# Optimization experiments

Measured on AMD Instinct MI355X. Metric: run time of the kernel, lower is better.

## Reference

```python
import jax, jax.numpy as jnp
import numpy as np

B, C, H, W = 8, 192, 120, 120
WSIZES = [4, 8, 12]
BN_EPS = 1e-5


def _conv1x1(t, w, b):
    # t: [b,c,h,w], w: [o,c], b: [o]
    return jnp.einsum('oc,bchw->bohw', w, t) + b[None, :, None, None]


def _bn(t, g, bb, m, v):
    scale = (g * jax.lax.rsqrt(v + BN_EPS))[None, :, None, None]
    return (t - m[None, :, None, None]) * scale + bb[None, :, None, None]


def _partition_qv(t, ws):
    # t: [b, 2c, h, w] -> qx, vx each [b*nh*nw, ws*ws, c]
    b, c2, h, w = t.shape
    c = c2 // 2
    nh, nw = h // ws, w // ws
    t = t.reshape(b, 2, c, nh, ws, nw, ws)
    t = t.transpose(1, 0, 3, 5, 4, 6, 2).reshape(2, b * nh * nw, ws * ws, c)
    return t[0], t[1]


def _merge(t, ws, b, h, w):
    # t: [b*nh*nw, ws*ws, c] -> [b, c, h, w]
    nh, nw = h // ws, w // ws
    c = t.shape[-1]
    t = t.reshape(b, nh, nw, ws, ws, c)
    return t.transpose(0, 5, 1, 3, 2, 4).reshape(b, c, h, w)


def setup_inputs() -> dict:
    key = jax.random.key(0)
    ks = jax.random.split(key, 6)
    d = {}
    d['x'] = jax.random.normal(ks[0], (B, C, H, W), jnp.float32)
    d['y'] = jax.random.normal(ks[1], (B, C, H, W), jnp.float32)
    d['w_in'] = jax.random.normal(ks[2], (2 * C, C), jnp.float32) * 0.05
    d['b_in'] = jax.random.normal(ks[3], (2 * C,), jnp.float32) * 0.01
    d['bn_gamma'] = jnp.ones((2 * C,), jnp.float32)
    d['bn_beta'] = jnp.zeros((2 * C,), jnp.float32)
    d['bn_mean'] = jnp.zeros((2 * C,), jnp.float32)
    d['bn_var'] = jnp.ones((2 * C,), jnp.float32)
    d['w_out'] = jax.random.normal(ks[4], (C, C), jnp.float32) * 0.05
    d['b_out'] = jax.random.normal(ks[5], (C,), jnp.float32) * 0.01
    return d


def reference(x, y, w_in, b_in, bn_gamma, bn_beta, bn_mean, bn_var, w_out, b_out):
    b, c, h, w = x.shape
    xp = _bn(_conv1x1(x, w_in, b_in), bn_gamma, bn_beta, bn_mean, bn_var)
    yp = _bn(_conv1x1(y, w_in, b_in), bn_gamma, bn_beta, bn_mean, bn_var)
    chunk = c * 2 // 3
    y1s, atns = [], []
    for i, ws in enumerate(WSIZES):
        x_ = xp[:, i * chunk:(i + 1) * chunk]
        y_ = yp[:, i * chunk:(i + 1) * chunk]
        s = ws // 2  # shifts > 0 -> shifted windows
        x_ = jnp.roll(x_, (-s, -s), axis=(2, 3))
        y_ = jnp.roll(y_, (-s, -s), axis=(2, 3))
        qx, vx = _partition_qv(x_, ws)
        qy, vy = _partition_qv(y_, ws)
        atn = jax.nn.softmax(jnp.einsum('nqc,nkc->nqk', qx, qy), axis=-1)
        o = jnp.einsum('nqk,nkc->nqc', atn, vx)
        o = _merge(o, ws, b, h, w)
        o = jnp.roll(o, (s, s), axis=(2, 3))
        y1s.append(o)
        atns.append(atn)
    y1 = _conv1x1(jnp.concatenate(y1s, axis=1), w_out, b_out)
    return (y1, atns[0], atns[1], atns[2])
```

## Files before the change

### kernel.cpp

```cpp
#include <hip/hip_runtime.h>

typedef __bf16 bf16x8 __attribute__((ext_vector_type(8)));
typedef float f32x4 __attribute__((ext_vector_type(4)));
typedef unsigned int u32x4 __attribute__((ext_vector_type(4)));
typedef unsigned int u32x2 __attribute__((ext_vector_type(2)));

#define HW 14400
#define CIN 192

__device__ __forceinline__ unsigned short f2bf(float f) {
  unsigned int u = __builtin_bit_cast(unsigned int, f);
  u = (u + 0x7FFFu + ((u >> 16) & 1u)) >> 16;
  return (unsigned short)u;
}
__device__ __forceinline__ float bf2f(unsigned short h) {
  unsigned int u = ((unsigned int)h) << 16;
  return __builtin_bit_cast(float, u);
}

__global__ void prep_kernel(const float* __restrict__ w_in, const float* __restrict__ b_in,
                            const float* __restrict__ g, const float* __restrict__ be,
                            const float* __restrict__ mu, const float* __restrict__ va,
                            const float* __restrict__ w_out,
                            unsigned short* __restrict__ wx, unsigned short* __restrict__ wy,
                            unsigned short* __restrict__ wo,
                            float* __restrict__ bx, float* __restrict__ by) {
  int idx = blockIdx.x * 256 + threadIdx.x;
  if (idx < 384 * 192) {
    int o = idx / 192;
    float s = g[o] * rsqrtf(va[o] + 1e-5f);
    wx[idx] = f2bf(w_in[idx] * s);
  } else if (idx < 384 * 192 + 192 * 192) {
    int j = idx - 384 * 192;
    int jo = j / 192, c = j % 192;
    int o = (jo >> 6) * 128 + (jo & 63);
    float s = g[o] * rsqrtf(va[o] + 1e-5f);
    wy[j] = f2bf(w_in[o * 192 + c] * s);
  } else if (idx < 384 * 192 + 2 * 192 * 192) {
    int j = idx - (384 * 192 + 192 * 192);
    wo[j] = f2bf(w_out[j]);
  }
  if (idx < 384) {
    float s = g[idx] * rsqrtf(va[idx] + 1e-5f);
    bx[idx] = (b_in[idx] - mu[idx]) * s + be[idx];
  } else if (idx < 384 + 192) {
    int jo = idx - 384;
    int o = (jo >> 6) * 128 + (jo & 63);
    float s = g[o] * rsqrtf(va[o] + 1e-5f);
    by[jo] = (b_in[o] - mu[o]) * s + be[o];
  }
}

template <int NOUT>
__launch_bounds__(256, 2)
__global__ void conv_in_kernel(const float* __restrict__ X,
                               const unsigned short* __restrict__ Wb,
                               const float* __restrict__ bias,
                               unsigned short* __restrict__ Out) {
  constexpr int NT = NOUT / 64;
  __shared__ unsigned short a_lds[64 * 40];
  __shared__ unsigned short b_lds[NOUT * 40];
  const int t = threadIdx.x;
  const int wave = t >> 6, lane = t & 63;
  const int l15 = lane & 15, l4 = lane >> 4;
  const int b = blockIdx.x / 225;
  const int px0 = (blockIdx.x % 225) * 64;
  const float* Xb = X + (size_t)b * CIN * HW + px0;
  const int wo0 = wave * (NOUT / 4);

  f32x4 acc[4][NT];
#pragma unroll
  for (int n = 0; n < NT; ++n) {
    float bv = bias[wo0 + n * 16 + l15];
    f32x4 iv = {bv, bv, bv, bv};
#pragma unroll
    for (int m = 0; m < 4; ++m) acc[m][n] = iv;
  }

  for (int kc = 0; kc < 6; ++kc) {
    const int c0 = kc * 32;
#pragma unroll
    for (int p = 0; p < 2; ++p) {
      int idx = p * 256 + t;
      int c = idx >> 4, px4 = (idx & 15) * 4;
      f32x4 v = *reinterpret_cast<const f32x4*>(Xb + (size_t)(c0 + c) * HW + px4);
      a_lds[(px4 + 0) * 40 + c] = f2bf(v[0]);
      a_lds[(px4 + 1) * 40 + c] = f2bf(v[1]);
      a_lds[(px4 + 2) * 40 + c] = f2bf(v[2]);
      a_lds[(px4 + 3) * 40 + c] = f2bf(v[3]);
    }
#pragma unroll
    for (int p = 0; p < NOUT / 64; ++p) {
      int o = p * 64 + (t >> 2), c8 = (t & 3) * 8;
      *reinterpret_cast<u32x4*>(&b_lds[o * 40 + c8]) =
          *reinterpret_cast<const u32x4*>(Wb + (size_t)o * CIN + c0 + c8);
    }
    __syncthreads();
    bf16x8 af[4];
#pragma unroll
    for (int m = 0; m < 4; ++m)
      af[m] = *reinterpret_cast<const bf16x8*>(&a_lds[(m * 16 + l15) * 40 + l4 * 8]);
#pragma unroll
    for (int n = 0; n < NT; ++n) {
      bf16x8 bfr = *reinterpret_cast<const bf16x8*>(&b_lds[(wo0 + n * 16 + l15) * 40 + l4 * 8]);
#pragma unroll
      for (int m = 0; m < 4; ++m)
        acc[m][n] = __builtin_amdgcn_mfma_f32_16x16x32_bf16(af[m], bfr, acc[m][n], 0, 0, 0);
    }
    __syncthreads();
  }

  unsigned short* Ob = Out + ((size_t)b * HW + px0) * NOUT;
#pragma unroll
  for (int m = 0; m < 4; ++m) {
#pragma unroll
    for (int r = 0; r < 4; ++r) {
      int px = m * 16 + l4 * 4 + r;
      unsigned short* dst = Ob + (size_t)px * NOUT + wo0 + l15;
#pragma unroll
      for (int n = 0; n < NT; ++n) dst[n * 16] = f2bf(acc[m][n][r]);
    }
  }
}

template <int WS, int SI, int NTHR>
__launch_bounds__(NTHR, 2)
__global__ void attn_kernel(const unsigned short* __restrict__ XP,
                            const unsigned short* __restrict__ YQ,
                            unsigned short* __restrict__ Z,
                            float* __restrict__ ATN) {
  constexpr int S = WS / 2, L = WS * WS, NH = 120 / WS, TT = L / 16;
  constexpr int NWAVE = NTHR / 64;
  constexpr int SMAX = (TT + NWAVE - 1) / NWAVE;
  constexpr int KP = ((L + 31) / 32) * 32;
  constexpr int PL = KP + 8;
  constexpr int KSTEPS = KP / 32;
  constexpr int POOLE = (L * 72 > L * PL) ? L * 72 : L * PL;
  __shared__ unsigned short pool[POOLE];
  __shared__ unsigned short vt_lds[64 * PL];
  unsigned short* k_lds = pool;
  unsigned short* p_lds = pool;

  const int t = threadIdx.x;
  const int win = blockIdx.x;
  const int b = win / (NH * NH);
  const int r_ = win % (NH * NH);
  const int ih = r_ / NH, iw = r_ % NH;
  const int wave = t >> 6, lane = t & 63, l15 = lane & 15, l4 = lane >> 4;

  auto pixof = [&](int e) {
    int p = e / WS, qc = e % WS;
    int h = ih * WS + p + S; if (h >= 120) h -= 120;
    int w = iw * WS + qc + S; if (w >= 120) w -= 120;
    return b * HW + h * 120 + w;
  };

  for (int idx = t; idx < L * 8; idx += NTHR) {
    int e = idx >> 3, c8 = (idx & 7) * 8;
    *reinterpret_cast<u32x4*>(&k_lds[e * 72 + c8]) =
        *reinterpret_cast<const u32x4*>(YQ + (size_t)pixof(e) * 192 + SI * 64 + c8);
  }
  for (int idx = t; idx < L * 8; idx += NTHR) {
    int e = idx >> 3, c8 = (idx & 7) * 8;
    u32x4 v = *reinterpret_cast<const u32x4*>(XP + (size_t)pixof(e) * 384 + SI * 128 + 64 + c8);
    const unsigned short* vh = reinterpret_cast<const unsigned short*>(&v);
#pragma unroll
    for (int j = 0; j < 8; ++j) vt_lds[(c8 + j) * PL + e] = vh[j];
  }
  if constexpr (KP > L) {
    for (int idx = t; idx < 64 * (KP - L); idx += NTHR)
      vt_lds[(idx / (KP - L)) * PL + L + (idx % (KP - L))] = 0;
  }

  bf16x8 af[SMAX][2];
#pragma unroll
  for (int si = 0; si < SMAX; ++si) {
    int ti = wave + si * NWAVE;
    if (ti < TT) {
      const unsigned short* qp =
          XP + (size_t)pixof(ti * 16 + l15) * 384 + SI * 128 + l4 * 8;
      af[si][0] = *reinterpret_cast<const bf16x8*>(qp);
      af[si][1] = *reinterpret_cast<const bf16x8*>(qp + 32);
    }
  }
  __syncthreads();

  f32x4 sacc[SMAX][TT];
#pragma unroll
  for (int si = 0; si < SMAX; ++si)
#pragma unroll
    for (int tj = 0; tj < TT; ++tj) sacc[si][tj] = f32x4{0.f, 0.f, 0.f, 0.f};
#pragma unroll
  for (int tj = 0; tj < TT; ++tj) {
    bf16x8 b0 = *reinterpret_cast<const bf16x8*>(&k_lds[(tj * 16 + l15) * 72 + l4 * 8]);
    bf16x8 b1 = *reinterpret_cast<const bf16x8*>(&k_lds[(tj * 16 + l15) * 72 + 32 + l4 * 8]);
#pragma unroll
    for (int si = 0; si < SMAX; ++si) {
      int ti = wave + si * NWAVE;
      if (ti < TT) {
        sacc[si][tj] = __builtin_amdgcn_mfma_f32_16x16x32_bf16(af[si][0], b0, sacc[si][tj], 0, 0, 0);
        sacc[si][tj] = __builtin_amdgcn_mfma_f32_16x16x32_bf16(af[si][1], b1, sacc[si][tj], 0, 0, 0);
      }
    }
  }

  float inv_[SMAX][4];
#pragma unroll
  for (int si = 0; si < SMAX; ++si) {
    int ti = wave + si * NWAVE;
    if (ti < TT) {
#pragma unroll
      for (int r = 0; r < 4; ++r) {
        float m = -1e30f;
#pragma unroll
        for (int tj = 0; tj < TT; ++tj) m = fmaxf(m, sacc[si][tj][r]);
#pragma unroll
        for (int mk = 1; mk < 16; mk <<= 1) m = fmaxf(m, __shfl_xor(m, mk, 64));
        float s = 0.f;
#pragma unroll
        for (int tj = 0; tj < TT; ++tj) {
          float e = __expf(sacc[si][tj][r] - m);
          sacc[si][tj][r] = e;
          s += e;
        }
#pragma unroll
        for (int mk = 1; mk < 16; mk <<= 1) s += __shfl_xor(s, mk, 64);
        inv_[si][r] = 1.f / s;
      }
    }
  }

  __syncthreads();

  if constexpr (KP > L) {
#pragma unroll
    for (int si = 0; si < SMAX; ++si) {
      int ti = wave + si * NWAVE;
      if (ti < TT)
        *reinterpret_cast<unsigned long long*>(
            &p_lds[(ti * 16 + l15) * PL + L + l4 * 4]) = 0ULL;
    }
  }

  float* aout = ATN + (size_t)win * L * L;
#pragma unroll
  for (int si = 0; si < SMAX; ++si) {
    int ti = wave + si * NWAVE;
    if (ti < TT) {
#pragma unroll
      for (int tj = 0; tj < TT; ++tj)
#pragma unroll
        for (int r = 0; r < 4; ++r) {
          float p = sacc[si][tj][r] * inv_[si][r];
          int row = ti * 16 + l4 * 4 + r, col = tj * 16 + l15;
          aout[row * L + col] = p;
          p_lds[row * PL + col] = f2bf(p);
        }
    }
  }
  __syncthreads();

#pragma unroll
  for (int si = 0; si < SMAX; ++si) {
    int ti = wave + si * NWAVE;
    if (ti < TT) {
      bf16x8 ap[KSTEPS];
#pragma unroll
      for (int kk = 0; kk < KSTEPS; ++kk)
        ap[kk] = *reinterpret_cast<const bf16x8*>(&p_lds[(ti * 16 + l15) * PL + kk * 32 + l4 * 8]);
      int opix[4];
#pragma unroll
      for (int r = 0; r < 4; ++r) opix[r] = pixof(ti * 16 + l4 * 4 + r);
#pragma unroll
      for (int cj = 0; cj < 4; ++cj) {
        f32x4 o = {0.f, 0.f, 0.f, 0.f};
#pragma unroll
        for (int kk = 0; kk < KSTEPS; ++kk) {
          bf16x8 bv = *reinterpret_cast<const bf16x8*>(&vt_lds[(cj * 16 + l15) * PL + kk * 32 + l4 * 8]);
          o = __builtin_amdgcn_mfma_f32_16x16x32_bf16(ap[kk], bv, o, 0, 0, 0);
        }
#pragma unroll
        for (int r = 0; r < 4; ++r)
          Z[(size_t)opix[r] * 192 + SI * 64 + cj * 16 + l15] = f2bf(o[r]);
      }
    }
  }
}

__launch_bounds__(256, 2)
__global__ void conv_out_kernel(const unsigned short* __restrict__ Z,
                                const unsigned short* __restrict__ Wo,
                                const float* __restrict__ bout,
                                float* __restrict__ Y1) {
  __shared__ unsigned short z_lds[64 * 40];
  __shared__ unsigned short w_lds[192 * 40];
  const int t = threadIdx.x, wave = t >> 6, lane = t & 63;
  const int l15 = lane & 15, l4 = lane >> 4;
  const int b = blockIdx.x / 225, px0 = (blockIdx.x % 225) * 64;
  const unsigned short* Zb = Z + ((size_t)b * HW + px0) * 192;
  const int wo0 = wave * 48;
  f32x4 acc[3][4];
#pragma unroll
  for (int m = 0; m < 3; ++m) {
    f32x4 bv;
#pragma unroll
    for (int r = 0; r < 4; ++r) bv[r] = bout[wo0 + m * 16 + l4 * 4 + r];
#pragma unroll
    for (int n = 0; n < 4; ++n) acc[m][n] = bv;
  }
  for (int kc = 0; kc < 6; ++kc) {
    const int c0 = kc * 32;
    {
      int px = t >> 2, c8 = (t & 3) * 8;
      *reinterpret_cast<u32x4*>(&z_lds[px * 40 + c8]) =
          *reinterpret_cast<const u32x4*>(Zb + (size_t)px * 192 + c0 + c8);
    }
#pragma unroll
    for (int p = 0; p < 3; ++p) {
      int o = p * 64 + (t >> 2), c8 = (t & 3) * 8;
      *reinterpret_cast<u32x4*>(&w_lds[o * 40 + c8]) =
          *reinterpret_cast<const u32x4*>(Wo + (size_t)o * 192 + c0 + c8);
    }
    __syncthreads();
    bf16x8 bfr[4];
#pragma unroll
    for (int n = 0; n < 4; ++n)
      bfr[n] = *reinterpret_cast<const bf16x8*>(&z_lds[(n * 16 + l15) * 40 + l4 * 8]);
#pragma unroll
    for (int m = 0; m < 3; ++m) {
      bf16x8 af = *reinterpret_cast<const bf16x8*>(&w_lds[(wo0 + m * 16 + l15) * 40 + l4 * 8]);
#pragma unroll
      for (int n = 0; n < 4; ++n)
        acc[m][n] = __builtin_amdgcn_mfma_f32_16x16x32_bf16(af, bfr[n], acc[m][n], 0, 0, 0);
    }
    __syncthreads();
  }
  float* Yb = Y1 + (size_t)b * 192 * HW + px0;
#pragma unroll
  for (int m = 0; m < 3; ++m) {
#pragma unroll
    for (int r = 0; r < 4; ++r) {
      int o = wo0 + m * 16 + l4 * 4 + r;
      float* dst = Yb + (size_t)o * HW + l15;
#pragma unroll
      for (int n = 0; n < 4; ++n) dst[n * 16] = acc[m][n][r];
    }
  }
}

extern "C" void kernel_launch(void* const* d_in, const int* in_sizes, int n_in,
                              void* d_out, int out_size, void* d_ws, size_t ws_size,
                              hipStream_t stream) {
  const float* x = (const float*)d_in[0];
  const float* y = (const float*)d_in[1];
  const float* w_in = (const float*)d_in[2];
  const float* b_in = (const float*)d_in[3];
  const float* g = (const float*)d_in[4];
  const float* be = (const float*)d_in[5];
  const float* mu = (const float*)d_in[6];
  const float* va = (const float*)d_in[7];
  const float* w_out = (const float*)d_in[8];
  const float* b_out = (const float*)d_in[9];
  char* ws = (char*)d_ws;
  unsigned short* wx = (unsigned short*)(ws + 0);
  unsigned short* wy = (unsigned short*)(ws + 147456);
  unsigned short* wo = (unsigned short*)(ws + 221184);
  float* bx = (float*)(ws + 294912);
  float* by = (float*)(ws + 296448);
  unsigned short* xp = (unsigned short*)(ws + 297216);
  unsigned short* yq = (unsigned short*)(ws + 297216 + (size_t)115200 * 384 * 2);
  unsigned short* z  = (unsigned short*)(ws + 297216 + (size_t)115200 * 384 * 2 +
                                         (size_t)115200 * 192 * 2);
  float* out = (float*)d_out;

  prep_kernel<<<576, 256, 0, stream>>>(w_in, b_in, g, be, mu, va, w_out, wx, wy, wo, bx, by);
  conv_in_kernel<384><<<1800, 256, 0, stream>>>(x, wx, bx, xp);
  conv_in_kernel<192><<<1800, 256, 0, stream>>>(y, wy, by, yq);
  attn_kernel<4, 0, 64><<<7200, 64, 0, stream>>>(xp, yq, z, out + 22118400);
  attn_kernel<8, 1, 256><<<1800, 256, 0, stream>>>(xp, yq, z, out + 23961600);
  attn_kernel<12, 2, 256><<<800, 256, 0, stream>>>(xp, yq, z, out + 31334400);
  conv_out_kernel<<<1800, 256, 0, stream>>>(z, wo, b_out, out);
}
```

Baseline: 225.5 us.

## Restructure conv kernels with permuted channel layout and batch ws4 attention windows

conv_in now runs 384 threads per block. It double-buffers the activation tile in LDS and reads weights straight from global into registers. Its output is stored as packed 8-byte writes, which permutes channels within each 64-channel group. The out-projection weights are permuted to match. The attention scores are unaffected because q and k share the same permutation, but this makes later kernels depend on the permuted layout. A new ws=4 attention kernel processes four windows per 256-thread block, one window per wave. conv_out drops the LDS staging of its operands and instead stages results through LDS so it can write coalesced float4 stores. Together these target LDS staging overhead, scattered 2-byte stores, and small-block launch inefficiency, at the cost of more registers and LDS per block.

```diff
diff --git a/kernel.cpp b/kernel.cpp
--- a/kernel.cpp
+++ b/kernel.cpp
@@ -2,6 +2,7 @@
 
 typedef __bf16 bf16x8 __attribute__((ext_vector_type(8)));
 typedef float f32x4 __attribute__((ext_vector_type(4)));
+typedef float f32x2 __attribute__((ext_vector_type(2)));
 typedef unsigned int u32x4 __attribute__((ext_vector_type(4)));
 typedef unsigned int u32x2 __attribute__((ext_vector_type(2)));
 
@@ -38,7 +39,10 @@
     wy[j] = f2bf(w_in[o * 192 + c] * s);
   } else if (idx < 384 * 192 + 2 * 192 * 192) {
     int j = idx - (384 * 192 + 192 * 192);
-    wo[j] = f2bf(w_out[j]);
+    int o = j / 192, cs = j % 192;
+    int s = cs & 63;
+    int src = (cs & ~63) | ((s & 3) * 16 + (s >> 2));
+    wo[j] = f2bf(w_out[o * 192 + src]);
   }
   if (idx < 384) {
     float s = g[idx] * rsqrtf(va[idx] + 1e-5f);
@@ -52,73 +56,85 @@
 }
 
 template <int NOUT>
-__launch_bounds__(256, 2)
+__launch_bounds__(384, 2)
 __global__ void conv_in_kernel(const float* __restrict__ X,
                                const unsigned short* __restrict__ Wb,
                                const float* __restrict__ bias,
                                unsigned short* __restrict__ Out) {
-  constexpr int NT = NOUT / 64;
-  __shared__ unsigned short a_lds[64 * 40];
-  __shared__ unsigned short b_lds[NOUT * 40];
+  constexpr int M = (NOUT == 384) ? 4 : 2;
+  __shared__ unsigned short a_lds[2][64 * 40];
   const int t = threadIdx.x;
-  const int wave = t >> 6, lane = t & 63;
-  const int l15 = lane & 15, l4 = lane >> 4;
+  const int wave = t >> 6, lane = t & 63, l15 = lane & 15, l4 = lane >> 4;
+  const int wchunk = (NOUT == 384) ? wave : (wave >> 1);
+  const int px_base = (NOUT == 384) ? 0 : ((wave & 1) * 32);
+  const int wo0 = wchunk * 64;
   const int b = blockIdx.x / 225;
   const int px0 = (blockIdx.x % 225) * 64;
   const float* Xb = X + (size_t)b * CIN * HW + px0;
-  const int wo0 = wave * (NOUT / 4);
-
-  f32x4 acc[4][NT];
-#pragma unroll
-  for (int n = 0; n < NT; ++n) {
+
+  f32x4 acc[M][4];
+#pragma unroll
+  for (int n = 0; n < 4; ++n) {
     float bv = bias[wo0 + n * 16 + l15];
-    f32x4 iv = {bv, bv, bv, bv};
-#pragma unroll
-    for (int m = 0; m < 4; ++m) acc[m][n] = iv;
-  }
+#pragma unroll
+    for (int m = 0; m < M; ++m) acc[m][n] = f32x4{bv, bv, bv, bv};
+  }
+
+  const int c_off = (t & 7) * 4, px2 = ((t >> 3) & 31) * 2;
+  auto stage = [&](int kc, int buf) {
+    if (t < 256) {
+      const float* src = Xb + (size_t)(kc * 32 + c_off) * HW + px2;
+      f32x2 v0 = *reinterpret_cast<const f32x2*>(src);
+      f32x2 v1 = *reinterpret_cast<const f32x2*>(src + HW);
+      f32x2 v2 = *reinterpret_cast<const f32x2*>(src + 2 * HW);
+      f32x2 v3 = *reinterpret_cast<const f32x2*>(src + 3 * HW);
+      u32x2 r0 = {(unsigned)f2bf(v0[0]) | ((unsigned)f2bf(v1[0]) << 16),
+                  (unsigned)f2bf(v2[0]) | ((unsigned)f2bf(v3[0]) << 16)};
+      u32x2 r1 = {(unsigned)f2bf(v0[1]) | ((unsigned)f2bf(v1[1]) << 16),
+                  (unsigned)f2bf(v2[1]) | ((unsigned)f2bf(v3[1]) << 16)};
+      *reinterpret_cast<u32x2*>(&a_lds[buf][px2 * 40 + c_off]) = r0;
+      *reinterpret_cast<u32x2*>(&a_lds[buf][(px2 + 1) * 40 + c_off]) = r1;
+    }
+  };
+  auto loadW = [&](int kc, int n) {
+    return *reinterpret_cast<const bf16x8*>(
+        Wb + (size_t)(wo0 + n * 16 + l15) * CIN + kc * 32 + l4 * 8);
+  };
+
+  stage(0, 0);
+  bf16x8 bw[4], bwn[4];
+#pragma unroll
+  for (int n = 0; n < 4; ++n) bw[n] = loadW(0, n);
 
   for (int kc = 0; kc < 6; ++kc) {
-    const int c0 = kc * 32;
-#pragma unroll
-    for (int p = 0; p < 2; ++p) {
-      int idx = p * 256 + t;
-      int c = idx >> 4, px4 = (idx & 15) * 4;
-      f32x4 v = *reinterpret_cast<const f32x4*>(Xb + (size_t)(c0 + c) * HW + px4);
-      a_lds[(px4 + 0) * 40 + c] = f2bf(v[0]);
-      a_lds[(px4 + 1) * 40 + c] = f2bf(v[1]);
-      a_lds[(px4 + 2) * 40 + c] = f2bf(v[2]);
-      a_lds[(px4 + 3) * 40 + c] = f2bf(v[3]);
-    }
-#pragma unroll
-    for (int p = 0; p < NOUT / 64; ++p) {
-      int o = p * 64 + (t >> 2), c8 = (t & 3) * 8;
-      *reinterpret_cast<u32x4*>(&b_lds[o * 40 + c8]) =
-          *reinterpret_cast<const u32x4*>(Wb + (size_t)o * CIN + c0 + c8);
-    }
     __syncthreads();
-    bf16x8 af[4];
-#pragma unroll
-    for (int m = 0; m < 4; ++m)
-      af[m] = *reinterpret_cast<const bf16x8*>(&a_lds[(m * 16 + l15) * 40 + l4 * 8]);
-#pragma unroll
-    for (int n = 0; n < NT; ++n) {
-      bf16x8 bfr = *reinterpret_cast<const bf16x8*>(&b_lds[(wo0 + n * 16 + l15) * 40 + l4 * 8]);
-#pragma unroll
-      for (int m = 0; m < 4; ++m)
-        acc[m][n] = __builtin_amdgcn_mfma_f32_16x16x32_bf16(af[m], bfr, acc[m][n], 0, 0, 0);
-    }
-    __syncthreads();
-  }
-
-  unsigned short* Ob = Out + ((size_t)b * HW + px0) * NOUT;
-#pragma unroll
-  for (int m = 0; m < 4; ++m) {
+    if (kc < 5) {
+      stage(kc + 1, (kc + 1) & 1);
+#pragma unroll
+      for (int n = 0; n < 4; ++n) bwn[n] = loadW(kc + 1, n);
+    }
+    bf16x8 af[M];
+#pragma unroll
+    for (int m = 0; m < M; ++m)
+      af[m] = *reinterpret_cast<const bf16x8*>(
+          &a_lds[kc & 1][(px_base + m * 16 + l15) * 40 + l4 * 8]);
+#pragma unroll
+    for (int n = 0; n < 4; ++n)
+#pragma unroll
+      for (int m = 0; m < M; ++m)
+        acc[m][n] = __builtin_amdgcn_mfma_f32_16x16x32_bf16(af[m], bw[n], acc[m][n], 0, 0, 0);
+#pragma unroll
+    for (int n = 0; n < 4; ++n) bw[n] = bwn[n];
+  }
+
+#pragma unroll
+  for (int m = 0; m < M; ++m) {
 #pragma unroll
     for (int r = 0; r < 4; ++r) {
-      int px = m * 16 + l4 * 4 + r;
-      unsigned short* dst = Ob + (size_t)px * NOUT + wo0 + l15;
-#pragma unroll
-      for (int n = 0; n < NT; ++n) dst[n * 16] = f2bf(acc[m][n][r]);
+      int px = px_base + m * 16 + l4 * 4 + r;
+      u32x2 pk = {(unsigned)f2bf(acc[m][0][r]) | ((unsigned)f2bf(acc[m][1][r]) << 16),
+                  (unsigned)f2bf(acc[m][2][r]) | ((unsigned)f2bf(acc[m][3][r]) << 16)};
+      *reinterpret_cast<u32x2*>(Out + ((size_t)b * HW + px0 + px) * NOUT + wo0 + l15 * 4) = pk;
     }
   }
 }
@@ -288,17 +304,105 @@
 }
 
 __launch_bounds__(256, 2)
+__global__ void attn4_kernel(const unsigned short* __restrict__ XP,
+                             const unsigned short* __restrict__ YQ,
+                             unsigned short* __restrict__ Z,
+                             float* __restrict__ ATN) {
+  __shared__ unsigned short kp[4][16 * 72];
+  __shared__ unsigned short vt[4][64 * 40];
+  const int t = threadIdx.x;
+  const int wave = t >> 6, lane = t & 63, l15 = lane & 15, l4 = lane >> 4;
+  const int win = blockIdx.x * 4 + wave;
+  const int b = win / 900;
+  const int r_ = win % 900;
+  const int ih = r_ / 30, iw = r_ % 30;
+  unsigned short* kl = kp[wave];
+  unsigned short* vtl = vt[wave];
+
+  auto pixof = [&](int e) {
+    int h = ih * 4 + (e >> 2) + 2; if (h >= 120) h -= 120;
+    int w = iw * 4 + (e & 3) + 2; if (w >= 120) w -= 120;
+    return b * HW + h * 120 + w;
+  };
+
+#pragma unroll
+  for (int it = 0; it < 2; ++it) {
+    int idx = it * 64 + lane;
+    int e = idx >> 3, c8 = (idx & 7) * 8;
+    *reinterpret_cast<u32x4*>(&kl[e * 72 + c8]) =
+        *reinterpret_cast<const u32x4*>(YQ + (size_t)pixof(e) * 192 + c8);
+    u32x4 v = *reinterpret_cast<const u32x4*>(XP + (size_t)pixof(e) * 384 + 64 + c8);
+    const unsigned short* vh = reinterpret_cast<const unsigned short*>(&v);
+#pragma unroll
+    for (int j = 0; j < 8; ++j) vtl[(c8 + j) * 40 + e] = vh[j];
+  }
+  {
+    u32x4 z4 = {0, 0, 0, 0};
+    *reinterpret_cast<u32x4*>(&vtl[lane * 40 + 16]) = z4;
+    *reinterpret_cast<u32x4*>(&vtl[lane * 40 + 24]) = z4;
+  }
+
+  const unsigned short* qp = XP + (size_t)pixof(l15) * 384 + l4 * 8;
+  bf16x8 af0 = *reinterpret_cast<const bf16x8*>(qp);
+  bf16x8 af1 = *reinterpret_cast<const bf16x8*>(qp + 32);
+
+  bf16x8 b0 = *reinterpret_cast<const bf16x8*>(&kl[l15 * 72 + l4 * 8]);
+  bf16x8 b1 = *reinterpret_cast<const bf16x8*>(&kl[l15 * 72 + 32 + l4 * 8]);
+  f32x4 sacc = {0.f, 0.f, 0.f, 0.f};
+  sacc = __builtin_amdgcn_mfma_f32_16x16x32_bf16(af0, b0, sacc, 0, 0, 0);
+  sacc = __builtin_amdgcn_mfma_f32_16x16x32_bf16(af1, b1, sacc, 0, 0, 0);
+
+  float inv_[4];
+#pragma unroll
+  for (int r = 0; r < 4; ++r) {
+    float m = sacc[r];
+#pragma unroll
+    for (int mk = 1; mk < 16; mk <<= 1) m = fmaxf(m, __shfl_xor(m, mk, 64));
+    float e = __expf(sacc[r] - m);
+    sacc[r] = e;
+    float s = e;
+#pragma unroll
+    for (int mk = 1; mk < 16; mk <<= 1) s += __shfl_xor(s, mk, 64);
+    inv_[r] = 1.f / s;
+  }
+
+  *reinterpret_cast<unsigned long long*>(&kl[l15 * 40 + 16 + l4 * 4]) = 0ULL;
+  float* aout = ATN + (size_t)win * 256;
+#pragma unroll
+  for (int r = 0; r < 4; ++r) {
+    float p = sacc[r] * inv_[r];
+    int row = l4 * 4 + r;
+    aout[row * 16 + l15] = p;
+    kl[row * 40 + l15] = f2bf(p);
+  }
+
+  bf16x8 ap = *reinterpret_cast<const bf16x8*>(&kl[l15 * 40 + l4 * 8]);
+  int opix[4];
+#pragma unroll
+  for (int r = 0; r < 4; ++r) opix[r] = pixof(l4 * 4 + r);
+#pragma unroll
+  for (int cj = 0; cj < 4; ++cj) {
+    bf16x8 bv = *reinterpret_cast<const bf16x8*>(&vtl[(cj * 16 + l15) * 40 + l4 * 8]);
+    f32x4 o = {0.f, 0.f, 0.f, 0.f};
+    o = __builtin_amdgcn_mfma_f32_16x16x32_bf16(ap, bv, o, 0, 0, 0);
+#pragma unroll
+    for (int r = 0; r < 4; ++r)
+      Z[(size_t)opix[r] * 192 + cj * 16 + l15] = f2bf(o[r]);
+  }
+}
+
+__launch_bounds__(256, 2)
 __global__ void conv_out_kernel(const unsigned short* __restrict__ Z,
                                 const unsigned short* __restrict__ Wo,
                                 const float* __restrict__ bout,
                                 float* __restrict__ Y1) {
-  __shared__ unsigned short z_lds[64 * 40];
-  __shared__ unsigned short w_lds[192 * 40];
+  __shared__ float ep[4][48 * 68];
   const int t = threadIdx.x, wave = t >> 6, lane = t & 63;
   const int l15 = lane & 15, l4 = lane >> 4;
   const int b = blockIdx.x / 225, px0 = (blockIdx.x % 225) * 64;
   const unsigned short* Zb = Z + ((size_t)b * HW + px0) * 192;
   const int wo0 = wave * 48;
+
   f32x4 acc[3][4];
 #pragma unroll
   for (int m = 0; m < 3; ++m) {
@@ -308,42 +412,43 @@
 #pragma unroll
     for (int n = 0; n < 4; ++n) acc[m][n] = bv;
   }
+
+#pragma unroll
   for (int kc = 0; kc < 6; ++kc) {
-    const int c0 = kc * 32;
-    {
-      int px = t >> 2, c8 = (t & 3) * 8;
-      *reinterpret_cast<u32x4*>(&z_lds[px * 40 + c8]) =
-          *reinterpret_cast<const u32x4*>(Zb + (size_t)px * 192 + c0 + c8);
-    }
-#pragma unroll
-    for (int p = 0; p < 3; ++p) {
-      int o = p * 64 + (t >> 2), c8 = (t & 3) * 8;
-      *reinterpret_cast<u32x4*>(&w_lds[o * 40 + c8]) =
-          *reinterpret_cast<const u32x4*>(Wo + (size_t)o * 192 + c0 + c8);
-    }
-    __syncthreads();
-    bf16x8 bfr[4];
+    bf16x8 aw[3], bz[4];
+#pragma unroll
+    for (int m = 0; m < 3; ++m)
+      aw[m] = *reinterpret_cast<const bf16x8*>(
+          Wo + (size_t)(wo0 + m * 16 + l15) * 192 + kc * 32 + l4 * 8);
 #pragma unroll
     for (int n = 0; n < 4; ++n)
-      bfr[n] = *reinterpret_cast<const bf16x8*>(&z_lds[(n * 16 + l15) * 40 + l4 * 8]);
-#pragma unroll
-    for (int m = 0; m < 3; ++m) {
-      bf16x8 af = *reinterpret_cast<const bf16x8*>(&w_lds[(wo0 + m * 16 + l15) * 40 + l4 * 8]);
+      bz[n] = *reinterpret_cast<const bf16x8*>(
+          Zb + (size_t)(n * 16 + l15) * 192 + kc * 32 + l4 * 8);
+#pragma unroll
+    for (int m = 0; m < 3; ++m)
 #pragma unroll
       for (int n = 0; n < 4; ++n)
-        acc[m][n] = __builtin_amdgcn_mfma_f32_16x16x32_bf16(af, bfr[n], acc[m][n], 0, 0, 0);
-    }
-    __syncthreads();
-  }
+        acc[m][n] = __builtin_amdgcn_mfma_f32_16x16x32_bf16(aw[m], bz[n], acc[m][n], 0, 0, 0);
+  }
+
+  float* sl = ep[wave];
+#pragma unroll
+  for (int m = 0; m < 3; ++m)
+#pragma unroll
+    for (int n = 0; n < 4; ++n)
+#pragma unroll
+      for (int r = 0; r < 4; ++r)
+        sl[(m * 16 + l4 * 4 + r) * 68 + n * 16 + l15] = acc[m][n][r];
+
   float* Yb = Y1 + (size_t)b * 192 * HW + px0;
 #pragma unroll
-  for (int m = 0; m < 3; ++m) {
-#pragma unroll
-    for (int r = 0; r < 4; ++r) {
-      int o = wo0 + m * 16 + l4 * 4 + r;
-      float* dst = Yb + (size_t)o * HW + l15;
-#pragma unroll
-      for (int n = 0; n < 4; ++n) dst[n * 16] = acc[m][n][r];
+  for (int i = 0; i < 3; ++i) {
+    int row = i * 16 + (lane >> 2);
+    int col0 = (lane & 3) * 16;
+#pragma unroll
+    for (int q = 0; q < 4; ++q) {
+      f32x4 vv = *reinterpret_cast<const f32x4*>(&sl[row * 68 + col0 + q * 4]);
+      *reinterpret_cast<f32x4*>(Yb + (size_t)(wo0 + row) * HW + col0 + q * 4) = vv;
     }
   }
 }
@@ -374,9 +479,9 @@
   float* out = (float*)d_out;
 
   prep_kernel<<<576, 256, 0, stream>>>(w_in, b_in, g, be, mu, va, w_out, wx, wy, wo, bx, by);
-  conv_in_kernel<384><<<1800, 256, 0, stream>>>(x, wx, bx, xp);
-  conv_in_kernel<192><<<1800, 256, 0, stream>>>(y, wy, by, yq);
-  attn_kernel<4, 0, 64><<<7200, 64, 0, stream>>>(xp, yq, z, out + 22118400);
+  conv_in_kernel<384><<<1800, 384, 0, stream>>>(x, wx, bx, xp);
+  conv_in_kernel<192><<<1800, 384, 0, stream>>>(y, wy, by, yq);
+  attn4_kernel<<<1800, 256, 0, stream>>>(xp, yq, z, out + 22118400);
   attn_kernel<8, 1, 256><<<1800, 256, 0, stream>>>(xp, yq, z, out + 23961600);
   attn_kernel<12, 2, 256><<<800, 256, 0, stream>>>(xp, yq, z, out + 31334400);
   conv_out_kernel<<<1800, 256, 0, stream>>>(z, wo, b_out, out);
```

Result: slower. 287.4 us (+27.4%).

## Double-buffer conv_in/conv_out staging, load weights to registers, vectorize output stores

Applied to the files above, without the earlier changes.

Both 1x1 conv GEMM kernels now use double-buffered LDS for the activation tile, with the next chunk's global loads prefetched into registers during the current MFMA step. Weight fragments are read straight from global memory into registers instead of being staged through LDS, which leaves one barrier per step. conv_in packs pairs of channels with v_cvt_pk_bf16_f32 and writes them with a rotated (swizzled) channel layout to reduce LDS bank conflicts. conv_out stages its results through a per-wave LDS buffer so the fp32 output is written with 16-byte coalesced stores, at the cost of extra shared memory that may lower occupancy.

```diff
diff --git a/kernel.cpp b/kernel.cpp
--- a/kernel.cpp
+++ b/kernel.cpp
@@ -16,6 +16,11 @@
 __device__ __forceinline__ float bf2f(unsigned short h) {
   unsigned int u = ((unsigned int)h) << 16;
   return __builtin_bit_cast(float, u);
+}
+__device__ __forceinline__ unsigned cvtpk(float lo, float hi) {
+  unsigned r;
+  asm("v_cvt_pk_bf16_f32 %0, %1, %2" : "=v"(r) : "v"(lo), "v"(hi));
+  return r;
 }
 
 __global__ void prep_kernel(const float* __restrict__ w_in, const float* __restrict__ b_in,
@@ -58,8 +63,7 @@
                                const float* __restrict__ bias,
                                unsigned short* __restrict__ Out) {
   constexpr int NT = NOUT / 64;
-  __shared__ unsigned short a_lds[64 * 40];
-  __shared__ unsigned short b_lds[NOUT * 40];
+  __shared__ unsigned short a_lds[2][64 * 40];
   const int t = threadIdx.x;
   const int wave = t >> 6, lane = t & 63;
   const int l15 = lane & 15, l4 = lane >> 4;
@@ -77,35 +81,51 @@
     for (int m = 0; m < 4; ++m) acc[m][n] = iv;
   }
 
+  const int c2 = (t >> 4) * 2, px4 = (t & 15) * 4;
+  const int rotS = (t & 3);
+  const int C2 = (c2 & 7) + 8 * (((c2 >> 3) + rotS) & 3);
+  f32x4 sv0, sv1;
+  auto stage_load = [&](int kc) {
+    sv0 = *reinterpret_cast<const f32x4*>(Xb + (size_t)(kc * 32 + c2) * HW + px4);
+    sv1 = *reinterpret_cast<const f32x4*>(Xb + (size_t)(kc * 32 + c2 + 1) * HW + px4);
+  };
+  auto stage_write = [&](int buf) {
+#pragma unroll
+    for (int j = 0; j < 4; ++j)
+      *reinterpret_cast<unsigned*>(&a_lds[buf][(px4 + j) * 40 + C2]) = cvtpk(sv0[j], sv1[j]);
+  };
+  auto loadW = [&](int kc, int n) {
+    return *reinterpret_cast<const bf16x8*>(
+        Wb + (size_t)(wo0 + n * 16 + l15) * CIN + kc * 32 + l4 * 8);
+  };
+  const int blkR = ((l4 + (l15 >> 2)) & 3) * 8;
+
+  bf16x8 bw[NT], bwn[NT];
+  stage_load(0);
+  stage_write(0);
+#pragma unroll
+  for (int n = 0; n < NT; ++n) bw[n] = loadW(0, n);
+  __syncthreads();
+
   for (int kc = 0; kc < 6; ++kc) {
-    const int c0 = kc * 32;
-#pragma unroll
-    for (int p = 0; p < 2; ++p) {
-      int idx = p * 256 + t;
-      int c = idx >> 4, px4 = (idx & 15) * 4;
-      f32x4 v = *reinterpret_cast<const f32x4*>(Xb + (size_t)(c0 + c) * HW + px4);
-      a_lds[(px4 + 0) * 40 + c] = f2bf(v[0]);
-      a_lds[(px4 + 1) * 40 + c] = f2bf(v[1]);
-      a_lds[(px4 + 2) * 40 + c] = f2bf(v[2]);
-      a_lds[(px4 + 3) * 40 + c] = f2bf(v[3]);
-    }
-#pragma unroll
-    for (int p = 0; p < NOUT / 64; ++p) {
-      int o = p * 64 + (t >> 2), c8 = (t & 3) * 8;
-      *reinterpret_cast<u32x4*>(&b_lds[o * 40 + c8]) =
-          *reinterpret_cast<const u32x4*>(Wb + (size_t)o * CIN + c0 + c8);
-    }
-    __syncthreads();
+    if (kc < 5) {
+      stage_load(kc + 1);
+#pragma unroll
+      for (int n = 0; n < NT; ++n) bwn[n] = loadW(kc + 1, n);
+    }
     bf16x8 af[4];
 #pragma unroll
     for (int m = 0; m < 4; ++m)
-      af[m] = *reinterpret_cast<const bf16x8*>(&a_lds[(m * 16 + l15) * 40 + l4 * 8]);
-#pragma unroll
-    for (int n = 0; n < NT; ++n) {
-      bf16x8 bfr = *reinterpret_cast<const bf16x8*>(&b_lds[(wo0 + n * 16 + l15) * 40 + l4 * 8]);
+      af[m] = *reinterpret_cast<const bf16x8*>(&a_lds[kc & 1][(m * 16 + l15) * 40 + blkR]);
+#pragma unroll
+    for (int n = 0; n < NT; ++n)
 #pragma unroll
       for (int m = 0; m < 4; ++m)
-        acc[m][n] = __builtin_amdgcn_mfma_f32_16x16x32_bf16(af[m], bfr, acc[m][n], 0, 0, 0);
+        acc[m][n] = __builtin_amdgcn_mfma_f32_16x16x32_bf16(af[m], bw[n], acc[m][n], 0, 0, 0);
+    if (kc < 5) {
+      stage_write((kc + 1) & 1);
+#pragma unroll
+      for (int n = 0; n < NT; ++n) bw[n] = bwn[n];
     }
     __syncthreads();
   }
@@ -292,13 +312,14 @@
                                 const unsigned short* __restrict__ Wo,
                                 const float* __restrict__ bout,
                                 float* __restrict__ Y1) {
-  __shared__ unsigned short z_lds[64 * 40];
-  __shared__ unsigned short w_lds[192 * 40];
+  __shared__ unsigned short z_lds[2][64 * 40];
+  __shared__ float ep[4][48 * 68];
   const int t = threadIdx.x, wave = t >> 6, lane = t & 63;
   const int l15 = lane & 15, l4 = lane >> 4;
   const int b = blockIdx.x / 225, px0 = (blockIdx.x % 225) * 64;
   const unsigned short* Zb = Z + ((size_t)b * HW + px0) * 192;
   const int wo0 = wave * 48;
+
   f32x4 acc[3][4];
 #pragma unroll
   for (int m = 0; m < 3; ++m) {
@@ -308,42 +329,68 @@
 #pragma unroll
     for (int n = 0; n < 4; ++n) acc[m][n] = bv;
   }
+
+  const int zpx = t >> 2, zc8 = (t & 3) * 8;
+  u32x4 zreg;
+  auto zload = [&](int kc) {
+    zreg = *reinterpret_cast<const u32x4*>(Zb + (size_t)zpx * 192 + kc * 32 + zc8);
+  };
+  auto zwrite = [&](int buf) {
+    *reinterpret_cast<u32x4*>(&z_lds[buf][zpx * 40 + zc8]) = zreg;
+  };
+  auto loadWo = [&](int kc, int m) {
+    return *reinterpret_cast<const bf16x8*>(
+        Wo + (size_t)(wo0 + m * 16 + l15) * 192 + kc * 32 + l4 * 8);
+  };
+
+  bf16x8 aw[3], awn[3];
+  zload(0);
+  zwrite(0);
+#pragma unroll
+  for (int m = 0; m < 3; ++m) aw[m] = loadWo(0, m);
+  __syncthreads();
+
   for (int kc = 0; kc < 6; ++kc) {
-    const int c0 = kc * 32;
-    {
-      int px = t >> 2, c8 = (t & 3) * 8;
-      *reinterpret_cast<u32x4*>(&z_lds[px * 40 + c8]) =
-          *reinterpret_cast<const u32x4*>(Zb + (size_t)px * 192 + c0 + c8);
-    }
-#pragma unroll
-    for (int p = 0; p < 3; ++p) {
-      int o = p * 64 + (t >> 2), c8 = (t & 3) * 8;
-      *reinterpret_cast<u32x4*>(&w_lds[o * 40 + c8]) =
-          *reinterpret_cast<const u32x4*>(Wo + (size_t)o * 192 + c0 + c8);
+    if (kc < 5) {
+      zload(kc + 1);
+#pragma unroll
+      for (int m = 0; m < 3; ++m) awn[m] = loadWo(kc + 1, m);
+    }
+    bf16x8 bz[4];
+#pragma unroll
+    for (int n = 0; n < 4; ++n)
+      bz[n] = *reinterpret_cast<const bf16x8*>(&z_lds[kc & 1][(n * 16 + l15) * 40 + l4 * 8]);
+#pragma unroll
+    for (int m = 0; m < 3; ++m)
+#pragma unroll
+      for (int n = 0; n < 4; ++n)
+        acc[m][n] = __builtin_amdgcn_mfma_f32_16x16x32_bf16(aw[m], bz[n], acc[m][n], 0, 0, 0);
+    if (kc < 5) {
+      zwrite((kc + 1) & 1);
+#pragma unroll
+      for (int m = 0; m < 3; ++m) aw[m] = awn[m];
     }
     __syncthreads();
-    bf16x8 bfr[4];
+  }
+
+  float* sl = ep[wave];
+#pragma unroll
+  for (int m = 0; m < 3; ++m)
 #pragma unroll
     for (int n = 0; n < 4; ++n)
-      bfr[n] = *reinterpret_cast<const bf16x8*>(&z_lds[(n * 16 + l15) * 40 + l4 * 8]);
-#pragma unroll
-    for (int m = 0; m < 3; ++m) {
-      bf16x8 af = *reinterpret_cast<const bf16x8*>(&w_lds[(wo0 + m * 16 + l15) * 40 + l4 * 8]);
-#pragma unroll
-      for (int n = 0; n < 4; ++n)
-        acc[m][n] = __builtin_amdgcn_mfma_f32_16x16x32_bf16(af, bfr[n], acc[m][n], 0, 0, 0);
-    }
-    __syncthreads();
-  }
+#pragma unroll
+      for (int r = 0; r < 4; ++r)
+        sl[(m * 16 + l4 * 4 + r) * 68 + n * 16 + l15] = acc[m][n][r];
+
   float* Yb = Y1 + (size_t)b * 192 * HW + px0;
 #pragma unroll
-  for (int m = 0; m < 3; ++m) {
-#pragma unroll
-    for (int r = 0; r < 4; ++r) {
-      int o = wo0 + m * 16 + l4 * 4 + r;
-      float* dst = Yb + (size_t)o * HW + l15;
-#pragma unroll
-      for (int n = 0; n < 4; ++n) dst[n * 16] = acc[m][n][r];
+  for (int i = 0; i < 3; ++i) {
+    int row = i * 16 + (lane >> 2);
+    int col0 = (lane & 3) * 16;
+#pragma unroll
+    for (int q = 0; q < 4; ++q) {
+      f32x4 vv = *reinterpret_cast<const f32x4*>(&sl[row * 68 + col0 + q * 4]);
+      *reinterpret_cast<f32x4*>(Yb + (size_t)(wo0 + row) * HW + col0 + q * 4) = vv;
     }
   }
 }
```

Result: slower. 248.3 us (+10.1%).

## Load conv weights directly into registers with prefetch, repad activation LDS tile

Applied to the files above, without the earlier changes.

The input 1x1 conv kernel stops staging weights through shared memory. Each wave now loads its weight fragments straight from global memory into registers and prefetches the next K-chunk while the current MFMAs run. The activation LDS tile is re-padded to a stride of 34 (17 dwords) and read with scalar dword loads, with each thread writing 2-pixel pairs, to reduce bank conflicts. The cost is more register pressure and redundant global weight reads across blocks, which rely on L2 caching.

```diff
diff --git a/kernel.cpp b/kernel.cpp
--- a/kernel.cpp
+++ b/kernel.cpp
@@ -2,6 +2,7 @@
 
 typedef __bf16 bf16x8 __attribute__((ext_vector_type(8)));
 typedef float f32x4 __attribute__((ext_vector_type(4)));
+typedef float f32x2 __attribute__((ext_vector_type(2)));
 typedef unsigned int u32x4 __attribute__((ext_vector_type(4)));
 typedef unsigned int u32x2 __attribute__((ext_vector_type(2)));
 
@@ -58,8 +59,7 @@
                                const float* __restrict__ bias,
                                unsigned short* __restrict__ Out) {
   constexpr int NT = NOUT / 64;
-  __shared__ unsigned short a_lds[64 * 40];
-  __shared__ unsigned short b_lds[NOUT * 40];
+  __shared__ unsigned short a_lds[64 * 34];
   const int t = threadIdx.x;
   const int wave = t >> 6, lane = t & 63;
   const int l15 = lane & 15, l4 = lane >> 4;
@@ -77,35 +77,55 @@
     for (int m = 0; m < 4; ++m) acc[m][n] = iv;
   }
 
+  auto loadW = [&](int kc, int n) {
+    return *reinterpret_cast<const bf16x8*>(
+        Wb + (size_t)(wo0 + n * 16 + l15) * CIN + kc * 32 + l4 * 8);
+  };
+
+  const int pxb2 = (t & 15) * 2;
+  const int cA = t >> 4;
+
+  bf16x8 bw[NT], bwn[NT];
+#pragma unroll
+  for (int n = 0; n < NT; ++n) bw[n] = loadW(0, n);
+
   for (int kc = 0; kc < 6; ++kc) {
-    const int c0 = kc * 32;
 #pragma unroll
     for (int p = 0; p < 2; ++p) {
-      int idx = p * 256 + t;
-      int c = idx >> 4, px4 = (idx & 15) * 4;
-      f32x4 v = *reinterpret_cast<const f32x4*>(Xb + (size_t)(c0 + c) * HW + px4);
-      a_lds[(px4 + 0) * 40 + c] = f2bf(v[0]);
-      a_lds[(px4 + 1) * 40 + c] = f2bf(v[1]);
-      a_lds[(px4 + 2) * 40 + c] = f2bf(v[2]);
-      a_lds[(px4 + 3) * 40 + c] = f2bf(v[3]);
-    }
-#pragma unroll
-    for (int p = 0; p < NOUT / 64; ++p) {
-      int o = p * 64 + (t >> 2), c8 = (t & 3) * 8;
-      *reinterpret_cast<u32x4*>(&b_lds[o * 40 + c8]) =
-          *reinterpret_cast<const u32x4*>(Wb + (size_t)o * CIN + c0 + c8);
+      int c = cA + p * 16;
+      const float* src = Xb + (size_t)(kc * 32 + c) * HW + pxb2;
+      f32x2 v0 = *reinterpret_cast<const f32x2*>(src);
+      f32x2 v1 = *reinterpret_cast<const f32x2*>(src + 32);
+      a_lds[(pxb2 + 0) * 34 + c] = f2bf(v0[0]);
+      a_lds[(pxb2 + 1) * 34 + c] = f2bf(v0[1]);
+      a_lds[(pxb2 + 32) * 34 + c] = f2bf(v1[0]);
+      a_lds[(pxb2 + 33) * 34 + c] = f2bf(v1[1]);
     }
     __syncthreads();
+    if (kc < 5) {
+#pragma unroll
+      for (int n = 0; n < NT; ++n) bwn[n] = loadW(kc + 1, n);
+    }
+    const unsigned int* lp = reinterpret_cast<const unsigned int*>(a_lds);
     bf16x8 af[4];
 #pragma unroll
-    for (int m = 0; m < 4; ++m)
-      af[m] = *reinterpret_cast<const bf16x8*>(&a_lds[(m * 16 + l15) * 40 + l4 * 8]);
-#pragma unroll
-    for (int n = 0; n < NT; ++n) {
-      bf16x8 bfr = *reinterpret_cast<const bf16x8*>(&b_lds[(wo0 + n * 16 + l15) * 40 + l4 * 8]);
+    for (int m = 0; m < 4; ++m) {
+      int base = (m * 16 + l15) * 17 + l4 * 4;
+      u32x4 u;
+      u[0] = lp[base + 0];
+      u[1] = lp[base + 1];
+      u[2] = lp[base + 2];
+      u[3] = lp[base + 3];
+      af[m] = __builtin_bit_cast(bf16x8, u);
+    }
+#pragma unroll
+    for (int n = 0; n < NT; ++n)
 #pragma unroll
       for (int m = 0; m < 4; ++m)
-        acc[m][n] = __builtin_amdgcn_mfma_f32_16x16x32_bf16(af[m], bfr, acc[m][n], 0, 0, 0);
+        acc[m][n] = __builtin_amdgcn_mfma_f32_16x16x32_bf16(af[m], bw[n], acc[m][n], 0, 0, 0);
+    if (kc < 5) {
+#pragma unroll
+      for (int n = 0; n < NT; ++n) bw[n] = bwn[n];
     }
     __syncthreads();
   }
```

Result: slower. 243.0 us (+7.7%).
